# Performance work log

Hardware: AMD Instinct MI355X
Metric: run time of the kernel (lower is better)

Reference implementation:

```python
import jax, jax.numpy as jnp
import numpy as np

N_POINTS = 1_000_000
N_DIM = 6
N_BINS = 128
AXIS = 0  # init kwarg: histogram along this phase-space coordinate
BANDWIDTH_REL = 1.0  # init kwarg: kernel width relative to bin width
_INV_SQRT2 = np.float32(0.7071067811865476)


def _ndtr(z):
    # Standard normal CDF
    return 0.5 * (1.0 + jax.lax.erf(z * _INV_SQRT2))


def setup_inputs() -> dict:
    key = jax.random.key(0)
    x = jax.random.normal(key, (N_POINTS, N_DIM), dtype=jnp.float32)
    bin_edges = jnp.linspace(-4.0, 4.0, N_BINS + 1, dtype=jnp.float32)
    return {"x": x, "bin_edges": bin_edges}


def reference(x, bin_edges):
    # KDE-based soft 1D histogram (Histogram1D.forward with kde=True).
    xa = x[:, AXIS]                              # (N,)
    resolution = bin_edges[1] - bin_edges[0]     # scalar bin width
    bandwidth = BANDWIDTH_REL * resolution
    # Gaussian CDF evaluated at every edge for every point: (N, B+1)
    cdf = _ndtr((bin_edges[None, :] - xa[:, None]) / bandwidth)
    # Per-point probability mass in each bin, averaged over points: (B,)
    hist = jnp.mean(cdf[:, 1:] - cdf[:, :-1], axis=0)
    # Normalize to a probability density over the binned range
    hist = hist / (jnp.sum(hist) * resolution)
    return hist
```

## Files before the change

### kernel.cpp

```cpp
#include <hip/hip_runtime.h>
#include <math.h>

#define NBINS  128
#define DFINE  2272
#define DOFF   118
#define GT_N   235
#define MAXNB  256
#define DPAD   2414

__global__ __launch_bounds__(256) void hist_kernel(const float* __restrict__ x,
                                                   const float* __restrict__ edges,
                                                   float* __restrict__ ws, int n, int nb) {
    __shared__ float D[DFINE];
    for (int i = threadIdx.x; i < DFINE; i += 256) D[i] = 0.0f;
    __syncthreads();

    const float e0 = edges[0];
    const float res = edges[1] - e0;
    const float sc = 16.0f / res;

    const int nth = nb * 256;
    for (int base = (blockIdx.x * 256 + threadIdx.x) * 4; base < n; base += nth * 4) {
        float xs[4];
        #pragma unroll
        for (int k = 0; k < 4; ++k) {
            int idx = base + k;
            xs[k] = (idx < n) ? x[(size_t)idx * 6] : -1.0e9f;
        }
        #pragma unroll
        for (int k = 0; k < 4; ++k) {
            float t16 = (xs[k] - e0) * sc;
            float fq = floorf(t16);
            int qf = (int)fq;
            if (qf < -117 || qf > 2148) continue;
            float s = t16 - fq;
            float s2 = s * s, s3 = s2 * s;
            float w0 = fmaf(-0.5f, s3, s2) - 0.5f * s;
            float w1 = fmaf(1.5f, s3, fmaf(-2.5f, s2, 1.0f));
            float w2 = fmaf(-1.5f, s3, fmaf(2.0f, s2, 0.5f * s));
            float w3 = fmaf(0.5f, s3, -0.5f * s2);
            int d = qf + DOFF;
            unsafeAtomicAdd(&D[d - 1], w0);
            unsafeAtomicAdd(&D[d],     w1);
            unsafeAtomicAdd(&D[d + 1], w2);
            unsafeAtomicAdd(&D[d + 2], w3);
        }
    }
    __syncthreads();
    float* slice = ws + (size_t)blockIdx.x * DFINE;
    for (int i = threadIdx.x; i < DFINE; i += 256) slice[i] = D[i];
}

__global__ __launch_bounds__(256) void reduce_kernel(const float* __restrict__ ws,
                                                     float* __restrict__ Dt, int nb) {
    int d = blockIdx.x * 256 + threadIdx.x;
    if (d >= DFINE) return;
    float a0 = 0.0f, a1 = 0.0f, a2 = 0.0f, a3 = 0.0f;
    int b = 0;
    for (; b + 4 <= nb; b += 4) {
        a0 += ws[(size_t)(b    ) * DFINE + d];
        a1 += ws[(size_t)(b + 1) * DFINE + d];
        a2 += ws[(size_t)(b + 2) * DFINE + d];
        a3 += ws[(size_t)(b + 3) * DFINE + d];
    }
    float acc = (a0 + a1) + (a2 + a3);
    for (; b < nb; ++b) acc += ws[(size_t)b * DFINE + d];
    Dt[d] = acc;
}

__global__ __launch_bounds__(128) void final_kernel(const float* __restrict__ Dt,
                                                    const float* __restrict__ edges,
                                                    float* __restrict__ out) {
    __shared__ float G[GT_N];
    __shared__ float Ds[DPAD];
    __shared__ float hs[NBINS];
    const int t = threadIdx.x;
    const float inv_sqrt2 = 0.70710678118654752440f;
    for (int k = t; k < GT_N; k += 128) {
        float u = (float)(k - 117) * 0.0625f;
        G[k] = 0.5f * (erff((u + 1.0f) * inv_sqrt2) - erff(u * inv_sqrt2));
    }
    for (int dd = t; dd < DFINE; dd += 128) Ds[dd + (dd >> 4)] = Dt[dd];
    __syncthreads();

    float acc = 0.0f;
    const int p0 = 16 * t;
    #pragma unroll 5
    for (int r = 1; r <= GT_N; ++r) {
        int idx = p0 + r;
        acc = fmaf(Ds[idx + (idx >> 4)], G[GT_N - r], acc);
    }
    hs[t] = acc;
    __syncthreads();
    for (int off = NBINS / 2; off >= 1; off >>= 1) {
        if (t < off) hs[t] += hs[t + off];
        __syncthreads();
    }
    float res = edges[1] - edges[0];
    out[t] = acc / (hs[0] * res);
}

extern "C" void kernel_launch(void* const* d_in, const int* in_sizes, int n_in,
                              void* d_out, int out_size, void* d_ws, size_t ws_size,
                              hipStream_t stream) {
    const float* x     = (const float*)d_in[0];
    const float* edges = (const float*)d_in[1];
    float* out = (float*)d_out;
    float* ws  = (float*)d_ws;
    int n = in_sizes[0] / 6;

    int nb = (int)(ws_size / (sizeof(float) * DFINE)) - 1;
    if (nb > MAXNB) nb = MAXNB;
    if (nb < 1) nb = 1;
    float* Dt = ws + (size_t)nb * DFINE;

    hist_kernel<<<nb, 256, 0, stream>>>(x, edges, ws, n, nb);
    reduce_kernel<<<(DFINE + 255) / 256, 256, 0, stream>>>(ws, Dt, nb);
    final_kernel<<<1, 128, 0, stream>>>(Dt, edges, out);
}
```

Baseline: 118.2 us.

## Raise histogram block cap and split cross-block reduction into partitions

Raises the maximum number of histogram blocks from 256 to 1024 so more CUs and waves work on the strided-gather/atomic phase. To keep the cross-block reduction from becoming a long serial chain, the reduce kernel now splits the block dimension into 8 interleaved partitions, producing 8 partial fine histograms. The final kernel sums these partials before the convolution. More blocks mean more workspace slices to write and read back, and the extra partial sum adds a little work in the single-block final kernel.

```diff
diff --git a/kernel.cpp b/kernel.cpp
--- a/kernel.cpp
+++ b/kernel.cpp
@@ -5,7 +5,8 @@
 #define DFINE  2272
 #define DOFF   118
 #define GT_N   235
-#define MAXNB  256
+#define NBMAX  1024
+#define NPART  8
 #define DPAD   2414
 
 __global__ __launch_bounds__(256) void hist_kernel(const float* __restrict__ x,
@@ -52,23 +53,25 @@
 }
 
 __global__ __launch_bounds__(256) void reduce_kernel(const float* __restrict__ ws,
-                                                     float* __restrict__ Dt, int nb) {
-    int d = blockIdx.x * 256 + threadIdx.x;
-    if (d >= DFINE) return;
+                                                     float* __restrict__ Pt, int nb) {
+    int gid = blockIdx.x * 256 + threadIdx.x;
+    if (gid >= DFINE * NPART) return;
+    int p = gid / DFINE;
+    int d = gid - p * DFINE;
     float a0 = 0.0f, a1 = 0.0f, a2 = 0.0f, a3 = 0.0f;
-    int b = 0;
-    for (; b + 4 <= nb; b += 4) {
-        a0 += ws[(size_t)(b    ) * DFINE + d];
-        a1 += ws[(size_t)(b + 1) * DFINE + d];
-        a2 += ws[(size_t)(b + 2) * DFINE + d];
-        a3 += ws[(size_t)(b + 3) * DFINE + d];
+    int b = p;
+    for (; b + 3 * NPART < nb; b += 4 * NPART) {
+        a0 += ws[(size_t)(b            ) * DFINE + d];
+        a1 += ws[(size_t)(b +     NPART) * DFINE + d];
+        a2 += ws[(size_t)(b + 2 * NPART) * DFINE + d];
+        a3 += ws[(size_t)(b + 3 * NPART) * DFINE + d];
     }
     float acc = (a0 + a1) + (a2 + a3);
-    for (; b < nb; ++b) acc += ws[(size_t)b * DFINE + d];
-    Dt[d] = acc;
+    for (; b < nb; b += NPART) acc += ws[(size_t)b * DFINE + d];
+    Pt[(size_t)p * DFINE + d] = acc;
 }
 
-__global__ __launch_bounds__(128) void final_kernel(const float* __restrict__ Dt,
+__global__ __launch_bounds__(128) void final_kernel(const float* __restrict__ Pt,
                                                     const float* __restrict__ edges,
                                                     float* __restrict__ out) {
     __shared__ float G[GT_N];
@@ -80,7 +83,12 @@
         float u = (float)(k - 117) * 0.0625f;
         G[k] = 0.5f * (erff((u + 1.0f) * inv_sqrt2) - erff(u * inv_sqrt2));
     }
-    for (int dd = t; dd < DFINE; dd += 128) Ds[dd + (dd >> 4)] = Dt[dd];
+    for (int dd = t; dd < DFINE; dd += 128) {
+        float v = 0.0f;
+        #pragma unroll
+        for (int p = 0; p < NPART; ++p) v += Pt[(size_t)p * DFINE + dd];
+        Ds[dd + (dd >> 4)] = v;
+    }
     __syncthreads();
 
     float acc = 0.0f;
@@ -109,12 +117,12 @@
     float* ws  = (float*)d_ws;
     int n = in_sizes[0] / 6;
 
-    int nb = (int)(ws_size / (sizeof(float) * DFINE)) - 1;
-    if (nb > MAXNB) nb = MAXNB;
+    int nb = (int)(ws_size / (sizeof(float) * DFINE)) - NPART;
+    if (nb > NBMAX) nb = NBMAX;
     if (nb < 1) nb = 1;
-    float* Dt = ws + (size_t)nb * DFINE;
+    float* Pt = ws + (size_t)nb * DFINE;
 
     hist_kernel<<<nb, 256, 0, stream>>>(x, edges, ws, n, nb);
-    reduce_kernel<<<(DFINE + 255) / 256, 256, 0, stream>>>(ws, Dt, nb);
-    final_kernel<<<1, 128, 0, stream>>>(Dt, edges, out);
+    reduce_kernel<<<(DFINE * NPART + 255) / 256, 256, 0, stream>>>(ws, Pt, nb);
+    final_kernel<<<1, 128, 0, stream>>>(Pt, edges, out);
 }
```

New measurement: 110.4 us. 6.6% less time.

## Replace per-block slice writes and reduce kernel with global atomics

Applied to the files above, without the earlier changes.

Each histogram block now adds its nonzero shared-memory bins directly into one global accumulator with atomics, instead of writing a full slice to workspace for a separate reduce kernel. A small zero kernel clears the accumulator first, and the grid is fixed at 512 blocks, up from at most 256. This removes the workspace round trip and the reduce launch, but adds contention on the global atomics and makes the float summation order nondeterministic.

```diff
diff --git a/kernel.cpp b/kernel.cpp
--- a/kernel.cpp
+++ b/kernel.cpp
@@ -5,12 +5,17 @@
 #define DFINE  2272
 #define DOFF   118
 #define GT_N   235
-#define MAXNB  256
+#define NB     512
 #define DPAD   2414
+
+__global__ __launch_bounds__(256) void zero_kernel(float* __restrict__ Dt) {
+    int i = blockIdx.x * 256 + threadIdx.x;
+    if (i < DFINE) Dt[i] = 0.0f;
+}
 
 __global__ __launch_bounds__(256) void hist_kernel(const float* __restrict__ x,
                                                    const float* __restrict__ edges,
-                                                   float* __restrict__ ws, int n, int nb) {
+                                                   float* __restrict__ Dt, int n) {
     __shared__ float D[DFINE];
     for (int i = threadIdx.x; i < DFINE; i += 256) D[i] = 0.0f;
     __syncthreads();
@@ -19,7 +24,7 @@
     const float res = edges[1] - e0;
     const float sc = 16.0f / res;
 
-    const int nth = nb * 256;
+    const int nth = NB * 256;
     for (int base = (blockIdx.x * 256 + threadIdx.x) * 4; base < n; base += nth * 4) {
         float xs[4];
         #pragma unroll
@@ -47,25 +52,10 @@
         }
     }
     __syncthreads();
-    float* slice = ws + (size_t)blockIdx.x * DFINE;
-    for (int i = threadIdx.x; i < DFINE; i += 256) slice[i] = D[i];
-}
-
-__global__ __launch_bounds__(256) void reduce_kernel(const float* __restrict__ ws,
-                                                     float* __restrict__ Dt, int nb) {
-    int d = blockIdx.x * 256 + threadIdx.x;
-    if (d >= DFINE) return;
-    float a0 = 0.0f, a1 = 0.0f, a2 = 0.0f, a3 = 0.0f;
-    int b = 0;
-    for (; b + 4 <= nb; b += 4) {
-        a0 += ws[(size_t)(b    ) * DFINE + d];
-        a1 += ws[(size_t)(b + 1) * DFINE + d];
-        a2 += ws[(size_t)(b + 2) * DFINE + d];
-        a3 += ws[(size_t)(b + 3) * DFINE + d];
+    for (int i = threadIdx.x; i < DFINE; i += 256) {
+        float v = D[i];
+        if (v != 0.0f) unsafeAtomicAdd(&Dt[i], v);
     }
-    float acc = (a0 + a1) + (a2 + a3);
-    for (; b < nb; ++b) acc += ws[(size_t)b * DFINE + d];
-    Dt[d] = acc;
 }
 
 __global__ __launch_bounds__(128) void final_kernel(const float* __restrict__ Dt,
@@ -80,7 +70,8 @@
         float u = (float)(k - 117) * 0.0625f;
         G[k] = 0.5f * (erff((u + 1.0f) * inv_sqrt2) - erff(u * inv_sqrt2));
     }
-    for (int dd = t; dd < DFINE; dd += 128) Ds[dd + (dd >> 4)] = Dt[dd];
+    for (int dd = t; dd < DFINE; dd += 128)
+        Ds[dd + (dd >> 4)] = Dt[dd];
     __syncthreads();
 
     float acc = 0.0f;
@@ -106,15 +97,10 @@
     const float* x     = (const float*)d_in[0];
     const float* edges = (const float*)d_in[1];
     float* out = (float*)d_out;
-    float* ws  = (float*)d_ws;
+    float* Dt  = (float*)d_ws;
     int n = in_sizes[0] / 6;
 
-    int nb = (int)(ws_size / (sizeof(float) * DFINE)) - 1;
-    if (nb > MAXNB) nb = MAXNB;
-    if (nb < 1) nb = 1;
-    float* Dt = ws + (size_t)nb * DFINE;
-
-    hist_kernel<<<nb, 256, 0, stream>>>(x, edges, ws, n, nb);
-    reduce_kernel<<<(DFINE + 255) / 256, 256, 0, stream>>>(ws, Dt, nb);
+    zero_kernel<<<(DFINE + 255) / 256, 256, 0, stream>>>(Dt);
+    hist_kernel<<<NB, 256, 0, stream>>>(x, edges, Dt, n);
     final_kernel<<<1, 128, 0, stream>>>(Dt, edges, out);
 }
```

After: 105.3 us. 11.0% less time.
